# Kernel optimization log

Hardware: AMD Instinct MI355X
Metric: run time of the kernel (lower is better)

Reference implementation:

```python
import jax, jax.numpy as jnp
import numpy as np

DIM = 512
HEADS = 8
D_HEAD = 64
INNER = HEADS * D_HEAD  # 512
CTX_DIM = 768
FF_INNER = 4 * DIM  # 2048
SCALE = D_HEAD ** -0.5
LN_EPS = 1e-5


def layer_norm(x, g, b):
    mu = jnp.mean(x, axis=-1, keepdims=True)
    var = jnp.var(x, axis=-1, keepdims=True)
    return (x - mu) * jax.lax.rsqrt(var + LN_EPS) * g + b


def attention(x, ctx, qw, kw, vw, ow, ob):
    B, N, _ = x.shape
    M = ctx.shape[1]
    q = (x @ qw).reshape(B, N, HEADS, D_HEAD).transpose(0, 2, 1, 3)
    k = (ctx @ kw).reshape(B, M, HEADS, D_HEAD).transpose(0, 2, 1, 3)
    v = (ctx @ vw).reshape(B, M, HEADS, D_HEAD).transpose(0, 2, 1, 3)
    sim = jnp.einsum('bhid,bhjd->bhij', q, k) * SCALE  # [B,H,N,M]
    attn = jax.nn.softmax(sim, axis=-1)
    out = jnp.einsum('bhij,bhjd->bhid', attn, v)
    out = out.transpose(0, 2, 1, 3).reshape(B, N, INNER)
    return out @ ow + ob


def setup_inputs() -> dict:
    key = jax.random.key(0)
    ks = jax.random.split(key, 20)
    r = lambda k, shp, s=0.02: jax.random.normal(k, shp, dtype=jnp.float32) * s
    return {
        'x': jax.random.normal(ks[0], (2, 4096, DIM), dtype=jnp.float32),
        'context': jax.random.normal(ks[1], (2, 256, CTX_DIM), dtype=jnp.float32),
        'q1_w': r(ks[2], (DIM, INNER)), 'k1_w': r(ks[3], (DIM, INNER)),
        'v1_w': r(ks[4], (DIM, INNER)), 'o1_w': r(ks[5], (INNER, DIM)),
        'o1_b': jnp.zeros((DIM,), jnp.float32),
        'q2_w': r(ks[6], (DIM, INNER)), 'k2_w': r(ks[7], (CTX_DIM, INNER)),
        'v2_w': r(ks[8], (CTX_DIM, INNER)), 'o2_w': r(ks[9], (INNER, DIM)),
        'o2_b': jnp.zeros((DIM,), jnp.float32),
        'ff_in_w': r(ks[10], (DIM, 2 * FF_INNER)), 'ff_in_b': jnp.zeros((2 * FF_INNER,), jnp.float32),
        'ff_out_w': r(ks[11], (FF_INNER, DIM)), 'ff_out_b': jnp.zeros((DIM,), jnp.float32),
        'ln1_g': jnp.ones((DIM,), jnp.float32), 'ln1_b': jnp.zeros((DIM,), jnp.float32),
        'ln2_g': jnp.ones((DIM,), jnp.float32), 'ln2_b': jnp.zeros((DIM,), jnp.float32),
        'ln3_g': jnp.ones((DIM,), jnp.float32), 'ln3_b': jnp.zeros((DIM,), jnp.float32),
    }


def reference(x, context, q1_w, k1_w, v1_w, o1_w, o1_b,
              q2_w, k2_w, v2_w, o2_w, o2_b,
              ff_in_w, ff_in_b, ff_out_w, ff_out_b,
              ln1_g, ln1_b, ln2_g, ln2_b, ln3_g, ln3_b):
    # self-attention + residual
    h = layer_norm(x, ln1_g, ln1_b)
    x = attention(h, h, q1_w, k1_w, v1_w, o1_w, o1_b) + x
    # cross-attention + residual
    h = layer_norm(x, ln2_g, ln2_b)
    x = attention(h, context, q2_w, k2_w, v2_w, o2_w, o2_b) + x
    # GEGLU feed-forward + residual (torch F.gelu is exact erf form)
    h = layer_norm(x, ln3_g, ln3_b)
    proj = h @ ff_in_w + ff_in_b
    val, gate = jnp.split(proj, 2, axis=-1)
    ff = (val * jax.nn.gelu(gate, approximate=False)) @ ff_out_w + ff_out_b
    return ff + x
```

## Files before the change

kernel.cpp:

```cpp
#include <hip/hip_runtime.h>
#include <hip/hip_bf16.h>
#include <cstdint>


typedef __bf16 bf16_t;
typedef __bf16 bf16x8 __attribute__((ext_vector_type(8)));
typedef float f32x4 __attribute__((ext_vector_type(4)));
typedef float f32x16 __attribute__((ext_vector_type(16)));

__device__ __forceinline__ bf16_t f2bf(float f) { return (bf16_t)f; }

__device__ __forceinline__ f32x4 mfma16(bf16x8 a, bf16x8 b, f32x4 c) {
  return __builtin_amdgcn_mfma_f32_16x16x32_bf16(a, b, c, 0, 0, 0);
}
__device__ __forceinline__ f32x16 mfma32(bf16x8 a, bf16x8 b, f32x16 c) {
  return __builtin_amdgcn_mfma_f32_32x32x16_bf16(a, b, c, 0, 0, 0);
}

__device__ __forceinline__ float gelu_exact(float x) {
  return 0.5f * x * (1.0f + erff(x * 0.70710678118654752f));
}

__device__ __forceinline__ void gload_lds16(const bf16_t* g, bf16_t* lds) {
  __builtin_amdgcn_global_load_lds(
      (const __attribute__((address_space(1))) unsigned int*)g,
      (__attribute__((address_space(3))) unsigned int*)lds, 16, 0, 0);
}

__global__ __launch_bounds__(256) void ln_kernel(const float* __restrict__ in,
                                                 const float* __restrict__ gw,
                                                 const float* __restrict__ bw,
                                                 bf16_t* __restrict__ out) {
  int w = threadIdx.x >> 6, l = threadIdx.x & 63;
  size_t row = (size_t)blockIdx.x * 4 + w;
  const float* p = in + row * 512 + l * 8;
  f32x4 va = *(const f32x4*)p;
  f32x4 vb = *(const f32x4*)(p + 4);
  float xs[8] = {va[0], va[1], va[2], va[3], vb[0], vb[1], vb[2], vb[3]};
  float s = 0.f;
#pragma unroll
  for (int j = 0; j < 8; j++) s += xs[j];
#pragma unroll
  for (int m = 1; m < 64; m <<= 1) s += __shfl_xor(s, m);
  float mu = s * (1.0f / 512.0f);
  float v = 0.f;
#pragma unroll
  for (int j = 0; j < 8; j++) { float d = xs[j] - mu; v += d * d; }
#pragma unroll
  for (int m = 1; m < 64; m <<= 1) v += __shfl_xor(v, m);
  float rstd = rsqrtf(v * (1.0f / 512.0f) + 1e-5f);
  f32x4 g0 = *(const f32x4*)(gw + l * 8);
  f32x4 g1 = *(const f32x4*)(gw + l * 8 + 4);
  f32x4 b0 = *(const f32x4*)(bw + l * 8);
  f32x4 b1 = *(const f32x4*)(bw + l * 8 + 4);
  bf16x8 o;
#pragma unroll
  for (int j = 0; j < 4; j++) o[j] = f2bf((xs[j] - mu) * rstd * g0[j] + b0[j]);
#pragma unroll
  for (int j = 0; j < 4; j++) o[4 + j] = f2bf((xs[4 + j] - mu) * rstd * g1[j] + b1[j]);
  *(bf16x8*)(out + row * 512 + l * 8) = o;
}

struct WJob {
  const float* W;
  bf16_t* Wt;
  int K;
  int N;
  float sc;
  int tile0;
};
struct WJobs {
  WJob j[10];
};

__global__ __launch_bounds__(256) void wtrans_all_kernel(WJobs jobs) {
  __shared__ float t[32][33];
  int bid = blockIdx.x;
  int i = 0;
#pragma unroll
  for (int q = 1; q < 10; q++)
    if (bid >= jobs.j[q].tile0) i = q;
  WJob jb = jobs.j[i];
  int tt = bid - jb.tile0;
  int ktiles = jb.K >> 5;
  int k0 = (tt % ktiles) * 32, n0 = (tt / ktiles) * 32;
#pragma unroll
  for (int s = 0; s < 4; s++) {
    int idx = threadIdx.x + s * 256;
    int kk = idx >> 5, nn = idx & 31;
    t[kk][nn] = jb.W[(size_t)(k0 + kk) * jb.N + n0 + nn];
  }
  __syncthreads();
#pragma unroll
  for (int s = 0; s < 4; s++) {
    int idx = threadIdx.x + s * 256;
    int nn = idx >> 5, kk = idx & 31;
    jb.Wt[(size_t)(n0 + nn) * jb.K + k0 + kk] = f2bf(t[kk][nn] * jb.sc);
  }
}

__global__ __launch_bounds__(256) void cvt_kernel(const float* __restrict__ in,
                                                  bf16_t* __restrict__ out) {
  int i = (blockIdx.x * 256 + threadIdx.x) * 4;
  f32x4 v = *(const f32x4*)(in + i);
  out[i + 0] = f2bf(v[0]);
  out[i + 1] = f2bf(v[1]);
  out[i + 2] = f2bf(v[2]);
  out[i + 3] = f2bf(v[3]);
}

template <int BM, int BN, int EPI>
__global__ __launch_bounds__(256) void gemm_kernel(
    const bf16_t* __restrict__ A, const bf16_t* __restrict__ Bt,
    const float* __restrict__ bias, const float* __restrict__ res,
    void* __restrict__ outp, int M, int N, int K, int gateOff, int ldo) {
  constexpr int WR = BM / 2;
  constexpr int WN = BN / 2;
  constexpr int MF = WR / 16;
  constexpr int NF = WN / 16;
  constexpr int ABLK = BM / 64;
  constexpr int BROWS = (EPI == 2) ? 2 * BN : BN;
  constexpr int BBLK = BROWS / 64;
  __shared__ bf16_t Al[2][2][BM][32];
  __shared__ bf16_t Bl[2][2][BROWS][32];

  int tid = threadIdx.x;
  int w = tid >> 6, l = tid & 63;
  int wr = w >> 1, wc = w & 1;
  int lg = l >> 4, lc = l & 15;
  int m0 = blockIdx.x * BM, n0 = blockIdx.y * BN;

  f32x4 acc[MF][NF] = {};
  f32x4 acc2[MF][NF] = {};

  int srow = tid >> 2, scol = (tid & 3) * 8;
  const bf16_t* aP[ABLK];
#pragma unroll
  for (int i = 0; i < ABLK; i++)
    aP[i] = A + (size_t)(m0 + i * 64 + srow) * K + scol;
  const bf16_t* bP[BBLK];
  if (EPI == 2) {
    bP[0] = Bt + (size_t)(n0 + srow) * K + scol;
    bP[1] = Bt + (size_t)(n0 + gateOff + srow) * K + scol;
  } else {
#pragma unroll
    for (int i = 0; i < BBLK; i++)
      bP[i] = Bt + (size_t)(n0 + i * 64 + srow) * K + scol;
  }

  auto STAGE = [&](int buf, int k0) {
#pragma unroll
    for (int kh = 0; kh < 2; kh++) {
#pragma unroll
      for (int i = 0; i < ABLK; i++)
        gload_lds16(aP[i] + k0 + kh * 32, &Al[buf][kh][i * 64 + w * 16][0]);
#pragma unroll
      for (int i = 0; i < BBLK; i++)
        gload_lds16(bP[i] + k0 + kh * 32, &Bl[buf][kh][i * 64 + w * 16][0]);
    }
  };

  int nk = K / 64;
  int cur = 0;
  STAGE(0, 0);
  __syncthreads();

  for (int t = 0; t < nk; ++t) {
    if (t + 1 < nk) STAGE(cur ^ 1, (t + 1) * 64);

#pragma unroll
    for (int kh = 0; kh < 2; kh++) {
      bf16x8 af[MF];
#pragma unroll
      for (int mi = 0; mi < MF; mi++)
        af[mi] = *(const bf16x8*)&Al[cur][kh][wr * WR + mi * 16 + lc][lg * 8];
      bf16x8 bfr[NF];
#pragma unroll
      for (int ni = 0; ni < NF; ni++)
        bfr[ni] = *(const bf16x8*)&Bl[cur][kh][wc * WN + ni * 16 + lc][lg * 8];
#pragma unroll
      for (int mi = 0; mi < MF; mi++)
#pragma unroll
        for (int ni = 0; ni < NF; ni++)
          acc[mi][ni] = mfma16(af[mi], bfr[ni], acc[mi][ni]);
      if (EPI == 2) {
        bf16x8 bg[NF];
#pragma unroll
        for (int ni = 0; ni < NF; ni++)
          bg[ni] =
              *(const bf16x8*)&Bl[cur][kh][BN + wc * WN + ni * 16 + lc][lg * 8];
#pragma unroll
        for (int mi = 0; mi < MF; mi++)
#pragma unroll
          for (int ni = 0; ni < NF; ni++)
            acc2[mi][ni] = mfma16(af[mi], bg[ni], acc2[mi][ni]);
      }
    }
    __syncthreads();
    cur ^= 1;
  }

#pragma unroll
  for (int mi = 0; mi < MF; mi++) {
#pragma unroll
    for (int ni = 0; ni < NF; ni++) {
#pragma unroll
      for (int r = 0; r < 4; r++) {
        int row = m0 + wr * WR + mi * 16 + lg * 4 + r;
        int col = n0 + wc * WN + ni * 16 + lc;
        float v = acc[mi][ni][r];
        if (EPI == 0) {
          ((bf16_t*)outp)[(size_t)row * ldo + col] = f2bf(v);
        } else if (EPI == 3) {
          int cs = (col & ~15) | (lc & 3) | ((lc & 4) << 1) | ((lc & 8) >> 1);
          ((bf16_t*)outp)[(size_t)row * ldo + cs] = f2bf(v);
        } else if (EPI == 1) {
          ((float*)outp)[(size_t)row * ldo + col] =
              v + bias[col] + res[(size_t)row * ldo + col];
        } else {
          float g = acc2[mi][ni][r] + bias[col + gateOff];
          float val = v + bias[col];
          ((bf16_t*)outp)[(size_t)row * ldo + col] = f2bf(val * gelu_exact(g));
        }
      }
    }
  }
}

__global__ __launch_bounds__(256) void attn_kernel(
    const bf16_t* __restrict__ Q, int ldq, const bf16_t* __restrict__ Kb,
    int ldk, const bf16_t* __restrict__ Vt, bf16_t* __restrict__ O, int Mkv) {
  __shared__ bf16_t Klds[64][72];
  __shared__ bf16_t Vlds[64][72];

  int lin = blockIdx.x;
  int xcd = lin & 7, slot = lin >> 3;
  int pair = 2 * xcd + (slot >> 5);
  int qt = slot & 31;
  int head = pair & 7, b = pair >> 3;

  int tid = threadIdx.x;
  int w = tid >> 6, l = tid & 63;
  int ql = l & 31, hi = l >> 5;
  int ldv = 2 * Mkv;

  size_t qrow = (size_t)b * 4096 + qt * 128 + w * 32 + ql;
  const bf16_t* qp = Q + qrow * ldq + head * 64 + hi * 8;
  bf16x8 qf[4];
#pragma unroll
  for (int dk = 0; dk < 4; dk++) qf[dk] = *(const bf16x8*)(qp + dk * 16);

  f32x16 o0 = {}, o1 = {};
  f32x16 zacc = {};
  float mrun = -1e30f;

  bf16x8 vones;
#pragma unroll
  for (int j = 0; j < 8; j++) vones[j] = f2bf(1.0f);

  int key0 = tid >> 2, dc0 = (tid & 3) * 16;
  const bf16_t* kp = Kb + ((size_t)b * Mkv + key0) * ldk + head * 64 + dc0;
  const bf16_t* vp = Vt + (size_t)(head * 64 + key0) * ldv + b * Mkv + dc0;

  bf16x8 kc0 = *(const bf16x8*)kp, kc1 = *(const bf16x8*)(kp + 8);
  bf16x8 vc0 = *(const bf16x8*)vp, vc1 = *(const bf16x8*)(vp + 8);

  for (int t0 = 0; t0 < Mkv; t0 += 64) {
    __syncthreads();
    *(bf16x8*)&Klds[key0][dc0] = kc0;
    *(bf16x8*)&Klds[key0][dc0 + 8] = kc1;
    *(bf16x8*)&Vlds[key0][dc0] = vc0;
    *(bf16x8*)&Vlds[key0][dc0 + 8] = vc1;
    __syncthreads();

    if (t0 + 64 < Mkv) {
      kp += (size_t)64 * ldk;
      vp += 64;
      kc0 = *(const bf16x8*)kp;
      kc1 = *(const bf16x8*)(kp + 8);
      vc0 = *(const bf16x8*)vp;
      vc1 = *(const bf16x8*)(vp + 8);
    }

    f32x16 s0 = {}, s1 = {};
    __builtin_amdgcn_s_setprio(1);
#pragma unroll
    for (int dk = 0; dk < 4; dk++) {
      bf16x8 a0 = *(const bf16x8*)&Klds[ql][dk * 16 + hi * 8];
      bf16x8 a1 = *(const bf16x8*)&Klds[32 + ql][dk * 16 + hi * 8];
      s0 = mfma32(a0, qf[dk], s0);
      s1 = mfma32(a1, qf[dk], s1);
    }
    __builtin_amdgcn_s_setprio(0);

    float tmax = s0[0];
#pragma unroll
    for (int r = 1; r < 16; r++) tmax = fmaxf(tmax, s0[r]);
#pragma unroll
    for (int r = 0; r < 16; r++) tmax = fmaxf(tmax, s1[r]);
    tmax = fmaxf(tmax, __shfl_xor(tmax, 32));

    if (!__all(tmax <= mrun + 8.0f)) {
      float mnew = fmaxf(mrun, tmax);
      float resc = __builtin_amdgcn_exp2f(mrun - mnew);
      mrun = mnew;
#pragma unroll
      for (int r = 0; r < 16; r++) {
        float f = __shfl(resc, (r & 3) + 8 * (r >> 2) + 4 * hi);
        o0[r] *= f;
        o1[r] *= f;
        zacc[r] *= f;
      }
    }

    bf16x8 pa[4];
#pragma unroll
    for (int m = 0; m < 4; m++) {
#pragma unroll
      for (int j = 0; j < 8; j++) {
        float sv = (m < 2) ? s0[(m & 1) * 8 + j] : s1[(m & 1) * 8 + j];
        pa[m][j] = f2bf(__builtin_amdgcn_exp2f(sv - mrun));
      }
    }

    __builtin_amdgcn_s_setprio(1);
#pragma unroll
    for (int m = 0; m < 4; m++) {
      zacc = mfma32(pa[m], vones, zacc);
      bf16x8 vb0 = *(const bf16x8*)&Vlds[ql][m * 16 + hi * 8];
      bf16x8 vb1 = *(const bf16x8*)&Vlds[32 + ql][m * 16 + hi * 8];
      o0 = mfma32(pa[m], vb0, o0);
      o1 = mfma32(pa[m], vb1, o1);
    }
    __builtin_amdgcn_s_setprio(0);
  }

  size_t ob = ((size_t)b * 4096 + qt * 128 + w * 32) * 512 + head * 64;
#pragma unroll
  for (int r = 0; r < 16; r++) {
    float inv = 1.0f / zacc[r];
    int q = (r & 3) + 8 * (r >> 2) + 4 * hi;
    O[ob + (size_t)q * 512 + ql] = f2bf(o0[r] * inv);
    O[ob + (size_t)q * 512 + 32 + ql] = f2bf(o1[r] * inv);
  }
}

extern "C" void kernel_launch(void* const* d_in, const int* in_sizes, int n_in,
                              void* d_out, int out_size, void* d_ws,
                              size_t ws_size, hipStream_t stream) {
  const float* x = (const float*)d_in[0];
  const float* ctx = (const float*)d_in[1];
  const float* q1_w = (const float*)d_in[2];
  const float* k1_w = (const float*)d_in[3];
  const float* v1_w = (const float*)d_in[4];
  const float* o1_w = (const float*)d_in[5];
  const float* o1_b = (const float*)d_in[6];
  const float* q2_w = (const float*)d_in[7];
  const float* k2_w = (const float*)d_in[8];
  const float* v2_w = (const float*)d_in[9];
  const float* o2_w = (const float*)d_in[10];
  const float* o2_b = (const float*)d_in[11];
  const float* ff_in_w = (const float*)d_in[12];
  const float* ff_in_b = (const float*)d_in[13];
  const float* ff_out_w = (const float*)d_in[14];
  const float* ff_out_b = (const float*)d_in[15];
  const float* ln1_g = (const float*)d_in[16];
  const float* ln1_b = (const float*)d_in[17];
  const float* ln2_g = (const float*)d_in[18];
  const float* ln2_b = (const float*)d_in[19];
  const float* ln3_g = (const float*)d_in[20];
  const float* ln3_b = (const float*)d_in[21];

  char* ws = (char*)d_ws;
  float* xr = (float*)(ws + 0);
  bf16_t* hb = (bf16_t*)(ws + 16777216);
  bf16_t* qkb = (bf16_t*)(ws + 25165824);
  bf16_t* ao = (bf16_t*)(ws + 41943040);
  bf16_t* ffmid = qkb;
  bf16_t* kb = (bf16_t*)(ws + 50331648);
  bf16_t* vtg2 = (bf16_t*)(ws + 50855936);
  bf16_t* ctxb = (bf16_t*)(ws + 51380224);
  bf16_t* wts = (bf16_t*)(ws + 58720256);
  bf16_t* vtg = (bf16_t*)(ws + 69730304);

  bf16_t* q1t = wts + 0;
  bf16_t* k1t = wts + 262144;
  bf16_t* v1t = wts + 524288;
  bf16_t* o1t = wts + 786432;
  bf16_t* q2t = wts + 1048576;
  bf16_t* k2t = wts + 1310720;
  bf16_t* v2t = wts + 1703936;
  bf16_t* o2t = wts + 2097152;
  bf16_t* ffint = wts + 2359296;
  bf16_t* ffoutt = wts + 4456448;

  const float QS = 0.125f * 1.44269504f;

  WJobs jobs;
  auto setj = [&](int i, const float* W, bf16_t* Wt, int K, int N, float sc,
                  int tile0) {
    jobs.j[i] = WJob{W, Wt, K, N, sc, tile0};
  };
  setj(0, q1_w, q1t, 512, 512, QS, 0);
  setj(1, k1_w, k1t, 512, 512, 1.0f, 256);
  setj(2, v1_w, v1t, 512, 512, 1.0f, 512);
  setj(3, o1_w, o1t, 512, 512, 1.0f, 768);
  setj(4, q2_w, q2t, 512, 512, QS, 1024);
  setj(5, k2_w, k2t, 768, 512, 1.0f, 1280);
  setj(6, v2_w, v2t, 768, 512, 1.0f, 1664);
  setj(7, o2_w, o2t, 512, 512, 1.0f, 2048);
  setj(8, ff_in_w, ffint, 512, 4096, 1.0f, 2304);
  setj(9, ff_out_w, ffoutt, 2048, 512, 1.0f, 4352);
  wtrans_all_kernel<<<5376, 256, 0, stream>>>(jobs);
  cvt_kernel<<<384, 256, 0, stream>>>(ctx, ctxb);

  ln_kernel<<<2048, 256, 0, stream>>>(x, ln1_g, ln1_b, hb);
  gemm_kernel<128, 128, 0><<<dim3(64, 8), 256, 0, stream>>>(
      hb, q1t, nullptr, nullptr, qkb, 8192, 1024, 512, 0, 1024);
  gemm_kernel<64, 128, 3><<<dim3(8, 64), 256, 0, stream>>>(
      v1t, hb, nullptr, nullptr, vtg, 512, 8192, 512, 0, 8192);
  attn_kernel<<<512, 256, 0, stream>>>(qkb, 1024, qkb + 512, 1024, vtg, ao,
                                       4096);
  gemm_kernel<64, 128, 1><<<dim3(128, 4), 256, 0, stream>>>(
      ao, o1t, o1_b, x, xr, 8192, 512, 512, 0, 512);

  ln_kernel<<<2048, 256, 0, stream>>>(xr, ln2_g, ln2_b, hb);
  gemm_kernel<64, 128, 0><<<dim3(128, 4), 256, 0, stream>>>(
      hb, q2t, nullptr, nullptr, qkb, 8192, 512, 512, 0, 512);
  gemm_kernel<64, 128, 0><<<dim3(8, 4), 256, 0, stream>>>(
      ctxb, k2t, nullptr, nullptr, kb, 512, 512, 768, 0, 512);
  gemm_kernel<64, 128, 3><<<dim3(8, 4), 256, 0, stream>>>(
      v2t, ctxb, nullptr, nullptr, vtg2, 512, 512, 768, 0, 512);
  attn_kernel<<<512, 256, 0, stream>>>(qkb, 512, kb, 512, vtg2, ao, 256);
  gemm_kernel<64, 128, 1><<<dim3(128, 4), 256, 0, stream>>>(
      ao, o2t, o2_b, xr, xr, 8192, 512, 512, 0, 512);

  ln_kernel<<<2048, 256, 0, stream>>>(xr, ln3_g, ln3_b, hb);
  gemm_kernel<128, 64, 2><<<dim3(64, 32), 256, 0, stream>>>(
      hb, ffint, ff_in_b, nullptr, ffmid, 8192, 2048, 512, 2048, 2048);
  gemm_kernel<64, 128, 1><<<dim3(128, 4), 256, 0, stream>>>(
      ffmid, ffoutt, ff_out_b, xr, (float*)d_out, 8192, 512, 2048, 0, 512);
}
```

Measured before the change: 305.4 us.

## Widen attention key tile to 128 and fuse cross-attn Q/K/V projections

The attention kernel now processes 128 keys per iteration instead of 64, computing four score tiles per step and interleaving exp with the PV MFMAs. This halves the number of barriers and online-softmax rescale checks per key. The three separate cross-attention projection GEMMs are merged into one launch, with a z dimension that routes blocks to Q, K or V work, removing two kernel launches. In exchange it uses more LDS and registers per block, and many z=1 blocks exit immediately.

```diff
diff --git a/kernel.cpp b/kernel.cpp
--- a/kernel.cpp
+++ b/kernel.cpp
@@ -227,11 +227,106 @@
   }
 }
 
+__global__ __launch_bounds__(256) void cross_fused_kernel(
+    const bf16_t* __restrict__ hb, const bf16_t* __restrict__ q2t,
+    bf16_t* __restrict__ qkb, const bf16_t* __restrict__ ctxb,
+    const bf16_t* __restrict__ k2t, bf16_t* __restrict__ kb,
+    const bf16_t* __restrict__ v2t, bf16_t* __restrict__ vtg2) {
+  constexpr int BM = 64, BN = 128;
+  constexpr int WR = 32, WN = 64, MF = 2, NF = 4;
+  __shared__ bf16_t Al[2][2][BM][32];
+  __shared__ bf16_t Bl[2][2][BN][32];
+
+  const bf16_t* A;
+  const bf16_t* Bt;
+  bf16_t* outp;
+  int K, m0;
+  bool perm = false;
+  if (blockIdx.z == 0) {
+    A = hb; Bt = q2t; outp = qkb; K = 512; m0 = blockIdx.x * BM;
+  } else {
+    int bx = blockIdx.x;
+    if (bx >= 16) return;
+    K = 768;
+    if (bx < 8) {
+      A = ctxb; Bt = k2t; outp = kb; m0 = bx * BM;
+    } else {
+      A = v2t; Bt = ctxb; outp = vtg2; perm = true; m0 = (bx - 8) * BM;
+    }
+  }
+  const int ldo = 512;
+  int n0 = blockIdx.y * BN;
+
+  int tid = threadIdx.x;
+  int w = tid >> 6, l = tid & 63;
+  int wr = w >> 1, wc = w & 1;
+  int lg = l >> 4, lc = l & 15;
+
+  f32x4 acc[MF][NF] = {};
+
+  int srow = tid >> 2, scol = (tid & 3) * 8;
+  const bf16_t* aP0 = A + (size_t)(m0 + srow) * K + scol;
+  const bf16_t* bP0 = Bt + (size_t)(n0 + srow) * K + scol;
+  const bf16_t* bP1 = Bt + (size_t)(n0 + 64 + srow) * K + scol;
+
+  auto STAGE = [&](int buf, int k0) {
+#pragma unroll
+    for (int kh = 0; kh < 2; kh++) {
+      gload_lds16(aP0 + k0 + kh * 32, &Al[buf][kh][w * 16][0]);
+      gload_lds16(bP0 + k0 + kh * 32, &Bl[buf][kh][w * 16][0]);
+      gload_lds16(bP1 + k0 + kh * 32, &Bl[buf][kh][64 + w * 16][0]);
+    }
+  };
+
+  int nk = K / 64;
+  int cur = 0;
+  STAGE(0, 0);
+  __syncthreads();
+
+  for (int t = 0; t < nk; ++t) {
+    if (t + 1 < nk) STAGE(cur ^ 1, (t + 1) * 64);
+#pragma unroll
+    for (int kh = 0; kh < 2; kh++) {
+      bf16x8 af[MF];
+#pragma unroll
+      for (int mi = 0; mi < MF; mi++)
+        af[mi] = *(const bf16x8*)&Al[cur][kh][wr * WR + mi * 16 + lc][lg * 8];
+      bf16x8 bfr[NF];
+#pragma unroll
+      for (int ni = 0; ni < NF; ni++)
+        bfr[ni] = *(const bf16x8*)&Bl[cur][kh][wc * WN + ni * 16 + lc][lg * 8];
+#pragma unroll
+      for (int mi = 0; mi < MF; mi++)
+#pragma unroll
+        for (int ni = 0; ni < NF; ni++)
+          acc[mi][ni] = mfma16(af[mi], bfr[ni], acc[mi][ni]);
+    }
+    __syncthreads();
+    cur ^= 1;
+  }
+
+#pragma unroll
+  for (int mi = 0; mi < MF; mi++) {
+#pragma unroll
+    for (int ni = 0; ni < NF; ni++) {
+#pragma unroll
+      for (int r = 0; r < 4; r++) {
+        int row = m0 + wr * WR + mi * 16 + lg * 4 + r;
+        int col = n0 + wc * WN + ni * 16 + lc;
+        int cs = perm ? ((col & ~15) | (lc & 3) | ((lc & 4) << 1) |
+                         ((lc & 8) >> 1))
+                      : col;
+        outp[(size_t)row * ldo + cs] = f2bf(acc[mi][ni][r]);
+      }
+    }
+  }
+}
+
 __global__ __launch_bounds__(256) void attn_kernel(
     const bf16_t* __restrict__ Q, int ldq, const bf16_t* __restrict__ Kb,
     int ldk, const bf16_t* __restrict__ Vt, bf16_t* __restrict__ O, int Mkv) {
-  __shared__ bf16_t Klds[64][72];
-  __shared__ bf16_t Vlds[64][72];
+  __shared__ bf16_t Klds[128][72];
+  __shared__ bf16_t Vlds[64][136];
 
   int lin = blockIdx.x;
   int xcd = lin & 7, slot = lin >> 3;
@@ -258,47 +353,67 @@
 #pragma unroll
   for (int j = 0; j < 8; j++) vones[j] = f2bf(1.0f);
 
-  int key0 = tid >> 2, dc0 = (tid & 3) * 16;
-  const bf16_t* kp = Kb + ((size_t)b * Mkv + key0) * ldk + head * 64 + dc0;
-  const bf16_t* vp = Vt + (size_t)(head * 64 + key0) * ldv + b * Mkv + dc0;
-
-  bf16x8 kc0 = *(const bf16x8*)kp, kc1 = *(const bf16x8*)(kp + 8);
-  bf16x8 vc0 = *(const bf16x8*)vp, vc1 = *(const bf16x8*)(vp + 8);
-
-  for (int t0 = 0; t0 < Mkv; t0 += 64) {
+  int krow = tid >> 1, kcc = (tid & 1) * 32;
+  int vrow = tid >> 2, vcc = (tid & 3) * 32;
+  const bf16_t* kp = Kb + ((size_t)b * Mkv + krow) * ldk + head * 64 + kcc;
+  const bf16_t* vp = Vt + (size_t)(head * 64 + vrow) * ldv + b * Mkv + vcc;
+
+  bf16x8 kr0 = *(const bf16x8*)kp, kr1 = *(const bf16x8*)(kp + 8);
+  bf16x8 kr2 = *(const bf16x8*)(kp + 16), kr3 = *(const bf16x8*)(kp + 24);
+  bf16x8 vr0 = *(const bf16x8*)vp, vr1 = *(const bf16x8*)(vp + 8);
+  bf16x8 vr2 = *(const bf16x8*)(vp + 16), vr3 = *(const bf16x8*)(vp + 24);
+
+  int nt = Mkv / 128;
+  for (int t = 0; t < nt; ++t) {
     __syncthreads();
-    *(bf16x8*)&Klds[key0][dc0] = kc0;
-    *(bf16x8*)&Klds[key0][dc0 + 8] = kc1;
-    *(bf16x8*)&Vlds[key0][dc0] = vc0;
-    *(bf16x8*)&Vlds[key0][dc0 + 8] = vc1;
+    *(bf16x8*)&Klds[krow][kcc] = kr0;
+    *(bf16x8*)&Klds[krow][kcc + 8] = kr1;
+    *(bf16x8*)&Klds[krow][kcc + 16] = kr2;
+    *(bf16x8*)&Klds[krow][kcc + 24] = kr3;
+    *(bf16x8*)&Vlds[vrow][vcc] = vr0;
+    *(bf16x8*)&Vlds[vrow][vcc + 8] = vr1;
+    *(bf16x8*)&Vlds[vrow][vcc + 16] = vr2;
+    *(bf16x8*)&Vlds[vrow][vcc + 24] = vr3;
     __syncthreads();
 
-    if (t0 + 64 < Mkv) {
-      kp += (size_t)64 * ldk;
-      vp += 64;
-      kc0 = *(const bf16x8*)kp;
-      kc1 = *(const bf16x8*)(kp + 8);
-      vc0 = *(const bf16x8*)vp;
-      vc1 = *(const bf16x8*)(vp + 8);
-    }
-
-    f32x16 s0 = {}, s1 = {};
+    if (t + 1 < nt) {
+      kp += (size_t)128 * ldk;
+      vp += 128;
+      kr0 = *(const bf16x8*)kp;
+      kr1 = *(const bf16x8*)(kp + 8);
+      kr2 = *(const bf16x8*)(kp + 16);
+      kr3 = *(const bf16x8*)(kp + 24);
+      vr0 = *(const bf16x8*)vp;
+      vr1 = *(const bf16x8*)(vp + 8);
+      vr2 = *(const bf16x8*)(vp + 16);
+      vr3 = *(const bf16x8*)(vp + 24);
+    }
+
+    f32x16 s0 = {}, s1 = {}, s2 = {}, s3 = {};
     __builtin_amdgcn_s_setprio(1);
 #pragma unroll
     for (int dk = 0; dk < 4; dk++) {
-      bf16x8 a0 = *(const bf16x8*)&Klds[ql][dk * 16 + hi * 8];
-      bf16x8 a1 = *(const bf16x8*)&Klds[32 + ql][dk * 16 + hi * 8];
+      int c = dk * 16 + hi * 8;
+      bf16x8 a0 = *(const bf16x8*)&Klds[ql][c];
+      bf16x8 a1 = *(const bf16x8*)&Klds[32 + ql][c];
+      bf16x8 a2 = *(const bf16x8*)&Klds[64 + ql][c];
+      bf16x8 a3 = *(const bf16x8*)&Klds[96 + ql][c];
       s0 = mfma32(a0, qf[dk], s0);
       s1 = mfma32(a1, qf[dk], s1);
+      s2 = mfma32(a2, qf[dk], s2);
+      s3 = mfma32(a3, qf[dk], s3);
     }
     __builtin_amdgcn_s_setprio(0);
 
-    float tmax = s0[0];
-#pragma unroll
-    for (int r = 1; r < 16; r++) tmax = fmaxf(tmax, s0[r]);
-#pragma unroll
-    for (int r = 0; r < 16; r++) tmax = fmaxf(tmax, s1[r]);
-    tmax = fmaxf(tmax, __shfl_xor(tmax, 32));
+    float tr[16];
+#pragma unroll
+    for (int r = 0; r < 16; r++)
+      tr[r] = fmaxf(fmaxf(s0[r], s1[r]), fmaxf(s2[r], s3[r]));
+#pragma unroll
+    for (int st = 8; st > 0; st >>= 1)
+#pragma unroll
+      for (int r = 0; r < st; r++) tr[r] = fmaxf(tr[r], tr[r + st]);
+    float tmax = fmaxf(tr[0], __shfl_xor(tr[0], 32));
 
     if (!__all(tmax <= mrun + 8.0f)) {
       float mnew = fmaxf(mrun, tmax);
@@ -313,24 +428,19 @@
       }
     }
 
-    bf16x8 pa[4];
-#pragma unroll
-    for (int m = 0; m < 4; m++) {
-#pragma unroll
-      for (int j = 0; j < 8; j++) {
-        float sv = (m < 2) ? s0[(m & 1) * 8 + j] : s1[(m & 1) * 8 + j];
-        pa[m][j] = f2bf(__builtin_amdgcn_exp2f(sv - mrun));
-      }
-    }
-
     __builtin_amdgcn_s_setprio(1);
 #pragma unroll
-    for (int m = 0; m < 4; m++) {
-      zacc = mfma32(pa[m], vones, zacc);
+    for (int m = 0; m < 8; m++) {
+      const f32x16 sm = (m < 2) ? s0 : (m < 4) ? s1 : (m < 6) ? s2 : s3;
+      bf16x8 pa;
+#pragma unroll
+      for (int j = 0; j < 8; j++)
+        pa[j] = f2bf(__builtin_amdgcn_exp2f(sm[(m & 1) * 8 + j] - mrun));
+      zacc = mfma32(pa, vones, zacc);
       bf16x8 vb0 = *(const bf16x8*)&Vlds[ql][m * 16 + hi * 8];
       bf16x8 vb1 = *(const bf16x8*)&Vlds[32 + ql][m * 16 + hi * 8];
-      o0 = mfma32(pa[m], vb0, o0);
-      o1 = mfma32(pa[m], vb1, o1);
+      o0 = mfma32(pa, vb0, o0);
+      o1 = mfma32(pa, vb1, o1);
     }
     __builtin_amdgcn_s_setprio(0);
   }
@@ -425,12 +535,8 @@
       ao, o1t, o1_b, x, xr, 8192, 512, 512, 0, 512);
 
   ln_kernel<<<2048, 256, 0, stream>>>(xr, ln2_g, ln2_b, hb);
-  gemm_kernel<64, 128, 0><<<dim3(128, 4), 256, 0, stream>>>(
-      hb, q2t, nullptr, nullptr, qkb, 8192, 512, 512, 0, 512);
-  gemm_kernel<64, 128, 0><<<dim3(8, 4), 256, 0, stream>>>(
-      ctxb, k2t, nullptr, nullptr, kb, 512, 512, 768, 0, 512);
-  gemm_kernel<64, 128, 3><<<dim3(8, 4), 256, 0, stream>>>(
-      v2t, ctxb, nullptr, nullptr, vtg2, 512, 512, 768, 0, 512);
+  cross_fused_kernel<<<dim3(128, 4, 2), 256, 0, stream>>>(
+      hb, q2t, qkb, ctxb, k2t, kb, v2t, vtg2);
   attn_kernel<<<512, 256, 0, stream>>>(qkb, 512, kb, 512, vtg2, ao, 256);
   gemm_kernel<64, 128, 1><<<dim3(128, 4), 256, 0, stream>>>(
       ao, o2t, o2_b, xr, xr, 8192, 512, 512, 0, 512);
```

Measured after the change: 327.3 us. +7.2%, slower.
